# Optimization experiments

Hardware: AMD Instinct MI355X
Metric: run time of the kernel (lower is better)

Reference implementation:

```python
import jax, jax.numpy as jnp
import numpy as np

T_ROIS = 200                       # TRAIN_ROIS_PER_IMAGE
POS_MAX = int(200 * 0.33)          # 66 max positives
R_RATIO = 1.0 / 0.33               # negative:positive ratio constant
MASK_SIZE = 28
BBOX_STD = np.array([0.1, 0.1, 0.2, 0.2], dtype=np.float32)


def _pairwise_iou(b1, b2):
    # b1 [N,4], b2 [G,4] -> [N,G]
    y1 = jnp.maximum(b1[:, None, 0], b2[None, :, 0])
    x1 = jnp.maximum(b1[:, None, 1], b2[None, :, 1])
    y2 = jnp.minimum(b1[:, None, 2], b2[None, :, 2])
    x2 = jnp.minimum(b1[:, None, 3], b2[None, :, 3])
    inter = jnp.maximum(x2 - x1, 0.0) * jnp.maximum(y2 - y1, 0.0)
    a1 = (b1[:, 2] - b1[:, 0]) * (b1[:, 3] - b1[:, 1])
    a2 = (b2[:, 2] - b2[:, 0]) * (b2[:, 3] - b2[:, 1])
    union = a1[:, None] + a2[None, :] - inter
    return jnp.where(union > 0, inter / jnp.where(union > 0, union, 1.0), 0.0)


def _box_refinement(box, gt):
    h = box[:, 2] - box[:, 0]
    w = box[:, 3] - box[:, 1]
    cy = box[:, 0] + 0.5 * h
    cx = box[:, 1] + 0.5 * w
    gh = gt[:, 2] - gt[:, 0]
    gw = gt[:, 3] - gt[:, 1]
    gcy = gt[:, 0] + 0.5 * gh
    gcx = gt[:, 1] + 0.5 * gw
    return jnp.stack([(gcy - cy) / h, (gcx - cx) / w,
                      jnp.log(gh / h), jnp.log(gw / w)], axis=1)


def _crop_and_resize(images, boxes, size):
    # TF tf.image.crop_and_resize (bilinear, extrapolation 0), images [K,H,W], boxes [K,4]
    K, H, W = images.shape
    y1, x1, y2, x2 = boxes[:, 0], boxes[:, 1], boxes[:, 2], boxes[:, 3]
    i = jnp.arange(size, dtype=images.dtype)
    ys = y1[:, None] * (H - 1) + i[None, :] * ((y2 - y1) * (H - 1) / (size - 1))[:, None]  # [K,S]
    xs = x1[:, None] * (W - 1) + i[None, :] * ((x2 - x1) * (W - 1) / (size - 1))[:, None]
    y0 = jnp.floor(ys)
    x0 = jnp.floor(xs)
    wy = (ys - y0)[:, :, None]   # [K,S,1]
    wx = (xs - x0)[:, None, :]   # [K,1,S]
    y0i = jnp.clip(y0, 0, H - 1).astype(jnp.int32)
    y1i = jnp.clip(y0 + 1, 0, H - 1).astype(jnp.int32)
    x0i = jnp.clip(x0, 0, W - 1).astype(jnp.int32)
    x1i = jnp.clip(x0 + 1, 0, W - 1).astype(jnp.int32)
    kk = jnp.arange(K)[:, None, None]
    v00 = images[kk, y0i[:, :, None], x0i[:, None, :]]
    v01 = images[kk, y0i[:, :, None], x1i[:, None, :]]
    v10 = images[kk, y1i[:, :, None], x0i[:, None, :]]
    v11 = images[kk, y1i[:, :, None], x1i[:, None, :]]
    val = (v00 * (1 - wx) + v01 * wx) * (1 - wy) + (v10 * (1 - wx) + v11 * wx) * wy
    ok = ((ys >= 0) & (ys <= H - 1))[:, :, None] & ((xs >= 0) & (xs <= W - 1))[:, None, :]
    return jnp.where(ok, val, 0.0)


def _detection_targets(proposals, gt_class_ids, gt_boxes, gt_masks):
    # proposals [N,4] f32, gt_class_ids [G] int32, gt_boxes [G,4] f32, gt_masks [H,W,G] bool
    valid_prop = jnp.sum(jnp.abs(proposals), axis=1) > 0          # trim_zeros (as mask)
    valid_gt = jnp.sum(jnp.abs(gt_boxes), axis=1) > 0
    is_crowd = valid_gt & (gt_class_ids < 0)
    is_fg = valid_gt & (gt_class_ids > 0)
    iou = _pairwise_iou(proposals, gt_boxes)                       # [N,G]
    iou = jnp.where(valid_prop[:, None], iou, 0.0)
    crowd_max = jnp.max(jnp.where(is_crowd[None, :], iou, 0.0), axis=1)
    no_crowd = crowd_max < 1e-3
    roi_iou_max = jnp.max(jnp.where(is_fg[None, :], iou, 0.0), axis=1)
    pos_bool = (roi_iou_max >= 0.5) & valid_prop
    neg_bool = (roi_iou_max < 0.5) & no_crowd & valid_prop
    num_pos = jnp.minimum(jnp.sum(pos_bool), POS_MAX)
    num_neg_want = jnp.floor(R_RATIO * num_pos.astype(jnp.float32)).astype(jnp.int32) - num_pos
    num_neg = jnp.clip(jnp.minimum(num_neg_want, jnp.sum(neg_bool)), 0, T_ROIS - num_pos)
    # deterministic subsample: lowest-index positives/negatives first (stable argsort)
    pos_order = jnp.argsort(jnp.logical_not(pos_bool))
    neg_order = jnp.argsort(jnp.logical_not(neg_bool))
    j = jnp.arange(T_ROIS)
    is_p = j < num_pos
    is_n = (j >= num_pos) & (j < num_pos + num_neg)
    sel = jnp.where(is_p, pos_order[j], neg_order[jnp.maximum(j - num_pos, 0)])
    keep = (is_p | is_n).astype(proposals.dtype)
    rois = proposals[sel] * keep[:, None]                          # zero-padded tail
    assign = jnp.argmax(jnp.where(is_fg[None, :], iou, -1.0)[sel], axis=1)
    class_ids = jnp.where(is_p, gt_class_ids[assign], 0)
    dummy = jnp.array([0.0, 0.0, 1.0, 1.0], dtype=proposals.dtype)  # safe box for padded rows
    p_roi = jnp.where(is_p[:, None], rois, dummy)
    p_gt = jnp.where(is_p[:, None], gt_boxes[assign], dummy)
    deltas = _box_refinement(p_roi, p_gt) / jnp.asarray(BBOX_STD)
    deltas = deltas * is_p[:, None]
    # mask targets: only first POS_MAX slots can be positive
    masks_t = jnp.transpose(gt_masks.astype(proposals.dtype), (2, 0, 1))   # [G,H,W]
    roi_m = masks_t[assign[:POS_MAX]]                              # [66,H,W]
    m = _crop_and_resize(roi_m, p_roi[:POS_MAX], MASK_SIZE)
    m = jnp.round(m) * is_p[:POS_MAX, None, None]
    masks = jnp.pad(m, ((0, T_ROIS - POS_MAX), (0, 0), (0, 0)))
    return rois, class_ids, deltas, masks


def _rand_boxes(k, shape):
    yx1 = jax.random.uniform(k, shape + (2,)) * 0.7
    hw = jax.random.uniform(jax.random.fold_in(k, 1), shape + (2,)) * 0.28 + 0.02
    return jnp.stack([yx1[..., 0], yx1[..., 1],
                      yx1[..., 0] + hw[..., 0], yx1[..., 1] + hw[..., 1]], axis=-1)


def setup_inputs() -> dict:
    key = jax.random.key(0)
    ks = jax.random.split(key, 6)
    B, N, G, H, W = 2, 2000, 100, 512, 512
    proposals = _rand_boxes(ks[0], (B, N))
    proposals = proposals * (jnp.arange(N) < int(N * 0.9))[None, :, None]  # zero-padded tail
    gt_boxes = _rand_boxes(ks[1], (B, G))
    gt_valid = jnp.arange(G) < 80
    gt_boxes = gt_boxes * gt_valid[None, :, None]
    cls = jax.random.randint(ks[2], (B, G), 1, 81).astype(jnp.int32)
    crowd = jax.random.uniform(ks[3], (B, G)) < 0.05
    cls = jnp.where(crowd, -cls, cls)
    cls = jnp.where(gt_valid[None, :], cls, 0)
    gt_masks = jax.random.randint(ks[4], (B, H, W, G), 0, 2).astype(bool)
    return {"proposals": proposals, "gt_class_ids": cls,
            "gt_boxes": gt_boxes, "gt_masks": gt_masks}


def reference(proposals, gt_class_ids, gt_boxes, gt_masks):
    return jax.vmap(_detection_targets)(proposals, gt_class_ids, gt_boxes, gt_masks)
```

## Files before the change

### kernel.cpp

```cpp
#include <hip/hip_runtime.h>
#include <math.h>

#define NPROP 2000
#define NGT   100
#define HH    512
#define WW    512
#define TR    200
#define PMAX  66
#define MS    28

__global__ __launch_bounds__(512) void k_select(
    const float* __restrict__ props,
    const int*   __restrict__ gcls,
    const float* __restrict__ gbox,
    float* __restrict__ out,
    int* __restrict__ wsi)
{
    const int b = blockIdx.x;
    const int t = threadIdx.x;
    const float* P  = props + (size_t)b * NPROP * 4;
    const float* GB = gbox  + (size_t)b * NGT * 4;
    const int*   GC = gcls  + (size_t)b * NGT;

    __shared__ float s_gb[NGT][4];
    __shared__ int   s_gc[NGT];
    __shared__ unsigned char s_fg[NGT], s_crowd[NGT];
    __shared__ float s_garea[NGT];
    __shared__ unsigned char s_pos[NPROP], s_neg[NPROP];
    __shared__ short s_assign[NPROP];
    __shared__ int s_selp[PMAX], s_seln[TR];
    __shared__ int s_wp[8], s_wn[8];
    __shared__ int s_totp, s_totn, s_np, s_nn;

    if (t < NGT) {
        float g0 = GB[t*4+0], g1 = GB[t*4+1], g2 = GB[t*4+2], g3 = GB[t*4+3];
        s_gb[t][0]=g0; s_gb[t][1]=g1; s_gb[t][2]=g2; s_gb[t][3]=g3;
        bool vg = (fabsf(g0)+fabsf(g1)+fabsf(g2)+fabsf(g3)) > 0.0f;
        int c = GC[t];
        s_gc[t] = c;
        s_fg[t]    = (unsigned char)(vg && (c > 0));
        s_crowd[t] = (unsigned char)(vg && (c < 0));
        s_garea[t] = __fmul_rn(__fsub_rn(g2,g0), __fsub_rn(g3,g1));
    }
    __syncthreads();

    for (int i = t; i < NPROP; i += 512) {
        float p0=P[i*4+0], p1=P[i*4+1], p2=P[i*4+2], p3=P[i*4+3];
        bool vp = (fabsf(p0)+fabsf(p1)+fabsf(p2)+fabsf(p3)) > 0.0f;
        float a1 = __fmul_rn(__fsub_rn(p2,p0), __fsub_rn(p3,p1));
        float crowd_max = 0.0f;
        float fgmax = 0.0f;
        float best = -INFINITY; int arg = 0;
        for (int g = 0; g < NGT; ++g) {
            float y1 = fmaxf(p0, s_gb[g][0]);
            float x1 = fmaxf(p1, s_gb[g][1]);
            float y2 = fminf(p2, s_gb[g][2]);
            float x2 = fminf(p3, s_gb[g][3]);
            float inter = __fmul_rn(fmaxf(__fsub_rn(x2,x1), 0.0f),
                                    fmaxf(__fsub_rn(y2,y1), 0.0f));
            float un = __fsub_rn(__fadd_rn(a1, s_garea[g]), inter);
            float iou = (un > 0.0f) ? __fdiv_rn(inter, un) : 0.0f;
            if (!vp) iou = 0.0f;
            if (s_crowd[g]) crowd_max = fmaxf(crowd_max, iou);
            float v;
            if (s_fg[g]) { fgmax = fmaxf(fgmax, iou); v = iou; }
            else         { v = -1.0f; }
            if (v > best) { best = v; arg = g; }
        }
        s_pos[i]    = (unsigned char)((fgmax >= 0.5f) && vp);
        s_neg[i]    = (unsigned char)((fgmax < 0.5f) && (crowd_max < 0.001f) && vp);
        s_assign[i] = (short)arg;
    }
    __syncthreads();

    int t4 = t * 4;
    int cp = 0, cn = 0;
    unsigned char lp[4], ln[4];
    #pragma unroll
    for (int e = 0; e < 4; ++e) {
        int i = t4 + e;
        unsigned char p = (i < NPROP) ? s_pos[i] : (unsigned char)0;
        unsigned char n = (i < NPROP) ? s_neg[i] : (unsigned char)0;
        lp[e] = p; ln[e] = n; cp += p; cn += n;
    }
    int ip = cp, inn = cn;
    int lane = t & 63;
    #pragma unroll
    for (int d = 1; d < 64; d <<= 1) {
        int vp2 = __shfl_up(ip, d);
        int vn2 = __shfl_up(inn, d);
        if (lane >= d) { ip += vp2; inn += vn2; }
    }
    if (lane == 63) { s_wp[t >> 6] = ip; s_wn[t >> 6] = inn; }
    __syncthreads();
    if (t == 0) {
        int ap = 0, an = 0;
        for (int w = 0; w < 8; ++w) {
            int tp = s_wp[w]; s_wp[w] = ap; ap += tp;
            int tn = s_wn[w]; s_wn[w] = an; an += tn;
        }
        s_totp = ap; s_totn = an;
    }
    __syncthreads();
    int ep = s_wp[t >> 6] + ip - cp;
    int en = s_wn[t >> 6] + inn - cn;
    #pragma unroll
    for (int e = 0; e < 4; ++e) {
        if (lp[e]) { if (ep < PMAX) s_selp[ep] = t4 + e; ep++; }
        if (ln[e]) { if (en < TR)   s_seln[en] = t4 + e; en++; }
    }
    __syncthreads();

    if (t == 0) {
        int np = min(s_totp, PMAX);
        const float R = (float)(1.0 / 0.33);
        int want = (int)floorf(__fmul_rn(R, (float)np)) - np;
        int nn = min(want, s_totn);
        nn = min(nn, TR - np);
        nn = max(nn, 0);
        s_np = np; s_nn = nn;
        wsi[b] = np;
    }
    __syncthreads();

    if (t < TR) {
        const int j = t;
        const int np = s_np, nn = s_nn;
        const bool isp  = j < np;
        const bool kept = j < np + nn;
        float r0=0, r1=0, r2=0, r3=0, cid=0, d0=0, d1=0, d2=0, d3=0;
        if (kept) {
            int sel = isp ? s_selp[j] : s_seln[j - np];
            r0 = P[sel*4+0]; r1 = P[sel*4+1]; r2 = P[sel*4+2]; r3 = P[sel*4+3];
            if (isp) {
                int g = (int)s_assign[sel];
                cid = (float)s_gc[g];
                float h  = __fsub_rn(r2, r0), w = __fsub_rn(r3, r1);
                float cy = __fadd_rn(r0, __fmul_rn(0.5f, h));
                float cx = __fadd_rn(r1, __fmul_rn(0.5f, w));
                float gh  = __fsub_rn(s_gb[g][2], s_gb[g][0]);
                float gw  = __fsub_rn(s_gb[g][3], s_gb[g][1]);
                float gcy = __fadd_rn(s_gb[g][0], __fmul_rn(0.5f, gh));
                float gcx = __fadd_rn(s_gb[g][1], __fmul_rn(0.5f, gw));
                d0 = __fdiv_rn(__fdiv_rn(__fsub_rn(gcy, cy), h), 0.1f);
                d1 = __fdiv_rn(__fdiv_rn(__fsub_rn(gcx, cx), w), 0.1f);
                d2 = __fdiv_rn(logf(__fdiv_rn(gh, h)), 0.2f);
                d3 = __fdiv_rn(logf(__fdiv_rn(gw, w)), 0.2f);
                if (j < PMAX) {
                    wsi[2 + b*PMAX + j] = g;
                    float* wsf = (float*)(wsi + 2 + 2*PMAX);
                    wsf[(b*PMAX + j)*4 + 0] = r0;
                    wsf[(b*PMAX + j)*4 + 1] = r1;
                    wsf[(b*PMAX + j)*4 + 2] = r2;
                    wsf[(b*PMAX + j)*4 + 3] = r3;
                }
            }
        }
        out[(size_t)b*TR*4 + j*4 + 0] = r0;
        out[(size_t)b*TR*4 + j*4 + 1] = r1;
        out[(size_t)b*TR*4 + j*4 + 2] = r2;
        out[(size_t)b*TR*4 + j*4 + 3] = r3;
        out[1600 + (size_t)b*TR + j] = cid;
        out[2000 + (size_t)b*TR*4 + j*4 + 0] = d0;
        out[2000 + (size_t)b*TR*4 + j*4 + 1] = d1;
        out[2000 + (size_t)b*TR*4 + j*4 + 2] = d2;
        out[2000 + (size_t)b*TR*4 + j*4 + 3] = d3;
    }
}

__global__ __launch_bounds__(256) void k_masks(
    const int* __restrict__ gmask,
    const int* __restrict__ wsi,
    float* __restrict__ out)
{
    const int bid = blockIdx.x;
    const int b = bid / TR, j = bid % TR;
    float* mout = out + 3600 + (size_t)b*TR*MS*MS + (size_t)j*MS*MS;
    const int np = wsi[b];
    if (j >= np) {
        for (int p = threadIdx.x; p < MS*MS; p += 256) mout[p] = 0.0f;
        return;
    }
    const int g = wsi[2 + b*PMAX + j];
    const float* wsf = (const float*)(wsi + 2 + 2*PMAX);
    const float y1 = wsf[(b*PMAX + j)*4 + 0];
    const float x1 = wsf[(b*PMAX + j)*4 + 1];
    const float y2 = wsf[(b*PMAX + j)*4 + 2];
    const float x2 = wsf[(b*PMAX + j)*4 + 3];

    const float sy = __fdiv_rn(__fmul_rn(__fsub_rn(y2, y1), 511.0f), 27.0f);
    const float sx = __fdiv_rn(__fmul_rn(__fsub_rn(x2, x1), 511.0f), 27.0f);
    const float by = __fmul_rn(y1, 511.0f);
    const float bx = __fmul_rn(x1, 511.0f);
    const int* GM = gmask + (size_t)b * HH * WW * NGT + g;

    for (int p = threadIdx.x; p < MS*MS; p += 256) {
        int iy = p / MS, ix = p % MS;
        float ys = __fadd_rn(by, __fmul_rn((float)iy, sy));
        float xs = __fadd_rn(bx, __fmul_rn((float)ix, sx));
        float y0f = floorf(ys), x0f = floorf(xs);
        float wy = __fsub_rn(ys, y0f);
        float wx = __fsub_rn(xs, x0f);
        int y0i = (int)fminf(fmaxf(y0f, 0.0f), 511.0f);
        int y1i = (int)fminf(fmaxf(__fadd_rn(y0f, 1.0f), 0.0f), 511.0f);
        int x0i = (int)fminf(fmaxf(x0f, 0.0f), 511.0f);
        int x1i = (int)fminf(fmaxf(__fadd_rn(x0f, 1.0f), 0.0f), 511.0f);
        float v00 = (float)GM[((size_t)y0i * WW + x0i) * NGT];
        float v01 = (float)GM[((size_t)y0i * WW + x1i) * NGT];
        float v10 = (float)GM[((size_t)y1i * WW + x0i) * NGT];
        float v11 = (float)GM[((size_t)y1i * WW + x1i) * NGT];
        float omwx = __fsub_rn(1.0f, wx), omwy = __fsub_rn(1.0f, wy);
        float top = __fadd_rn(__fmul_rn(v00, omwx), __fmul_rn(v01, wx));
        float bot = __fadd_rn(__fmul_rn(v10, omwx), __fmul_rn(v11, wx));
        float val = __fadd_rn(__fmul_rn(top, omwy), __fmul_rn(bot, wy));
        bool ok = (ys >= 0.0f) && (ys <= 511.0f) && (xs >= 0.0f) && (xs <= 511.0f);
        val = ok ? val : 0.0f;
        mout[p] = rintf(val);
    }
}

extern "C" void kernel_launch(void* const* d_in, const int* in_sizes, int n_in,
                              void* d_out, int out_size, void* d_ws, size_t ws_size,
                              hipStream_t stream) {
    const float* props = (const float*)d_in[0];
    const int*   gcls  = (const int*)  d_in[1];
    const float* gbox  = (const float*)d_in[2];
    const int*   gmask = (const int*)  d_in[3];
    float* out = (float*)d_out;
    int* wsi = (int*)d_ws;

    k_select<<<2, 512, 0, stream>>>(props, gcls, gbox, out, wsi);
    k_masks<<<2 * TR, 256, 0, stream>>>(gmask, wsi, out);
}
```

Before: 325.9 us.

## Split IoU flag computation into a separate multi-block kernel before selection

The per-proposal IoU and flag computation moves out of the 2-block select kernel into a new kernel launched on an 8x2 grid of 256-thread blocks. Each proposal's pos/neg flags and assigned GT index are packed into one int in workspace. A smaller pick kernel then reads these flags to run the scan and compaction, and reads GT boxes and classes from global memory. This spreads the 100-GT IoU loop over 16 blocks instead of 2, at the cost of one extra kernel launch and a workspace round-trip.

```diff
diff --git a/kernel.cpp b/kernel.cpp
--- a/kernel.cpp
+++ b/kernel.cpp
@@ -8,8 +8,64 @@
 #define TR    200
 #define PMAX  66
 #define MS    28
-
-__global__ __launch_bounds__(512) void k_select(
+#define FLAGS_OFF 4096
+
+__global__ __launch_bounds__(256) void k_flags(
+    const float* __restrict__ props,
+    const int*   __restrict__ gcls,
+    const float* __restrict__ gbox,
+    int* __restrict__ wsi)
+{
+    const int b = blockIdx.y;
+    const int i = blockIdx.x * 256 + threadIdx.x;
+    const float* P  = props + (size_t)b * NPROP * 4;
+    const float* GB = gbox  + (size_t)b * NGT * 4;
+    const int*   GC = gcls  + (size_t)b * NGT;
+
+    __shared__ float s_gb[NGT][4];
+    __shared__ float s_garea[NGT];
+    __shared__ unsigned char s_fg[NGT], s_crowd[NGT];
+
+    if (threadIdx.x < NGT) {
+        int t = threadIdx.x;
+        float g0 = GB[t*4+0], g1 = GB[t*4+1], g2 = GB[t*4+2], g3 = GB[t*4+3];
+        s_gb[t][0]=g0; s_gb[t][1]=g1; s_gb[t][2]=g2; s_gb[t][3]=g3;
+        bool vg = (fabsf(g0)+fabsf(g1)+fabsf(g2)+fabsf(g3)) > 0.0f;
+        int c = GC[t];
+        s_fg[t]    = (unsigned char)(vg && (c > 0));
+        s_crowd[t] = (unsigned char)(vg && (c < 0));
+        s_garea[t] = __fmul_rn(__fsub_rn(g2,g0), __fsub_rn(g3,g1));
+    }
+    __syncthreads();
+
+    if (i >= NPROP) return;
+    float p0=P[i*4+0], p1=P[i*4+1], p2=P[i*4+2], p3=P[i*4+3];
+    bool vp = (fabsf(p0)+fabsf(p1)+fabsf(p2)+fabsf(p3)) > 0.0f;
+    float a1 = __fmul_rn(__fsub_rn(p2,p0), __fsub_rn(p3,p1));
+    float crowd_max = 0.0f, fgmax = 0.0f;
+    float best = -INFINITY; int arg = 0;
+    for (int g = 0; g < NGT; ++g) {
+        float y1 = fmaxf(p0, s_gb[g][0]);
+        float x1 = fmaxf(p1, s_gb[g][1]);
+        float y2 = fminf(p2, s_gb[g][2]);
+        float x2 = fminf(p3, s_gb[g][3]);
+        float inter = __fmul_rn(fmaxf(__fsub_rn(x2,x1), 0.0f),
+                                fmaxf(__fsub_rn(y2,y1), 0.0f));
+        float un = __fsub_rn(__fadd_rn(a1, s_garea[g]), inter);
+        float iou = (un > 0.0f) ? __fdiv_rn(inter, un) : 0.0f;
+        if (!vp) iou = 0.0f;
+        if (s_crowd[g]) crowd_max = fmaxf(crowd_max, iou);
+        float v;
+        if (s_fg[g]) { fgmax = fmaxf(fgmax, iou); v = iou; }
+        else         { v = -1.0f; }
+        if (v > best) { best = v; arg = g; }
+    }
+    int pos = (int)((fgmax >= 0.5f) && vp);
+    int neg = (int)((fgmax < 0.5f) && (crowd_max < 0.001f) && vp);
+    wsi[FLAGS_OFF + b*NPROP + i] = pos | (neg << 1) | (arg << 2);
+}
+
+__global__ __launch_bounds__(512) void k_pick(
     const float* __restrict__ props,
     const int*   __restrict__ gcls,
     const float* __restrict__ gbox,
@@ -21,67 +77,19 @@
     const float* P  = props + (size_t)b * NPROP * 4;
     const float* GB = gbox  + (size_t)b * NGT * 4;
     const int*   GC = gcls  + (size_t)b * NGT;
-
-    __shared__ float s_gb[NGT][4];
-    __shared__ int   s_gc[NGT];
-    __shared__ unsigned char s_fg[NGT], s_crowd[NGT];
-    __shared__ float s_garea[NGT];
-    __shared__ unsigned char s_pos[NPROP], s_neg[NPROP];
-    __shared__ short s_assign[NPROP];
-    __shared__ int s_selp[PMAX], s_seln[TR];
+    const int*   F  = wsi + FLAGS_OFF + b * NPROP;
+
+    __shared__ int s_selp[PMAX], s_seln[TR], s_selpg[PMAX];
     __shared__ int s_wp[8], s_wn[8];
     __shared__ int s_totp, s_totn, s_np, s_nn;
 
-    if (t < NGT) {
-        float g0 = GB[t*4+0], g1 = GB[t*4+1], g2 = GB[t*4+2], g3 = GB[t*4+3];
-        s_gb[t][0]=g0; s_gb[t][1]=g1; s_gb[t][2]=g2; s_gb[t][3]=g3;
-        bool vg = (fabsf(g0)+fabsf(g1)+fabsf(g2)+fabsf(g3)) > 0.0f;
-        int c = GC[t];
-        s_gc[t] = c;
-        s_fg[t]    = (unsigned char)(vg && (c > 0));
-        s_crowd[t] = (unsigned char)(vg && (c < 0));
-        s_garea[t] = __fmul_rn(__fsub_rn(g2,g0), __fsub_rn(g3,g1));
-    }
-    __syncthreads();
-
-    for (int i = t; i < NPROP; i += 512) {
-        float p0=P[i*4+0], p1=P[i*4+1], p2=P[i*4+2], p3=P[i*4+3];
-        bool vp = (fabsf(p0)+fabsf(p1)+fabsf(p2)+fabsf(p3)) > 0.0f;
-        float a1 = __fmul_rn(__fsub_rn(p2,p0), __fsub_rn(p3,p1));
-        float crowd_max = 0.0f;
-        float fgmax = 0.0f;
-        float best = -INFINITY; int arg = 0;
-        for (int g = 0; g < NGT; ++g) {
-            float y1 = fmaxf(p0, s_gb[g][0]);
-            float x1 = fmaxf(p1, s_gb[g][1]);
-            float y2 = fminf(p2, s_gb[g][2]);
-            float x2 = fminf(p3, s_gb[g][3]);
-            float inter = __fmul_rn(fmaxf(__fsub_rn(x2,x1), 0.0f),
-                                    fmaxf(__fsub_rn(y2,y1), 0.0f));
-            float un = __fsub_rn(__fadd_rn(a1, s_garea[g]), inter);
-            float iou = (un > 0.0f) ? __fdiv_rn(inter, un) : 0.0f;
-            if (!vp) iou = 0.0f;
-            if (s_crowd[g]) crowd_max = fmaxf(crowd_max, iou);
-            float v;
-            if (s_fg[g]) { fgmax = fmaxf(fgmax, iou); v = iou; }
-            else         { v = -1.0f; }
-            if (v > best) { best = v; arg = g; }
-        }
-        s_pos[i]    = (unsigned char)((fgmax >= 0.5f) && vp);
-        s_neg[i]    = (unsigned char)((fgmax < 0.5f) && (crowd_max < 0.001f) && vp);
-        s_assign[i] = (short)arg;
-    }
-    __syncthreads();
-
     int t4 = t * 4;
-    int cp = 0, cn = 0;
-    unsigned char lp[4], ln[4];
+    int fl[4]; int cp = 0, cn = 0;
     #pragma unroll
     for (int e = 0; e < 4; ++e) {
         int i = t4 + e;
-        unsigned char p = (i < NPROP) ? s_pos[i] : (unsigned char)0;
-        unsigned char n = (i < NPROP) ? s_neg[i] : (unsigned char)0;
-        lp[e] = p; ln[e] = n; cp += p; cn += n;
+        fl[e] = (i < NPROP) ? F[i] : 0;
+        cp += (fl[e] & 1); cn += ((fl[e] >> 1) & 1);
     }
     int ip = cp, inn = cn;
     int lane = t & 63;
@@ -106,8 +114,8 @@
     int en = s_wn[t >> 6] + inn - cn;
     #pragma unroll
     for (int e = 0; e < 4; ++e) {
-        if (lp[e]) { if (ep < PMAX) s_selp[ep] = t4 + e; ep++; }
-        if (ln[e]) { if (en < TR)   s_seln[en] = t4 + e; en++; }
+        if (fl[e] & 1) { if (ep < PMAX) { s_selp[ep] = t4 + e; s_selpg[ep] = (fl[e] >> 2) & 127; } ep++; }
+        if ((fl[e] >> 1) & 1) { if (en < TR) s_seln[en] = t4 + e; en++; }
     }
     __syncthreads();
 
@@ -133,15 +141,16 @@
             int sel = isp ? s_selp[j] : s_seln[j - np];
             r0 = P[sel*4+0]; r1 = P[sel*4+1]; r2 = P[sel*4+2]; r3 = P[sel*4+3];
             if (isp) {
-                int g = (int)s_assign[sel];
-                cid = (float)s_gc[g];
+                int g = s_selpg[j];
+                cid = (float)GC[g];
+                float gb0 = GB[g*4+0], gb1 = GB[g*4+1], gb2 = GB[g*4+2], gb3 = GB[g*4+3];
                 float h  = __fsub_rn(r2, r0), w = __fsub_rn(r3, r1);
                 float cy = __fadd_rn(r0, __fmul_rn(0.5f, h));
                 float cx = __fadd_rn(r1, __fmul_rn(0.5f, w));
-                float gh  = __fsub_rn(s_gb[g][2], s_gb[g][0]);
-                float gw  = __fsub_rn(s_gb[g][3], s_gb[g][1]);
-                float gcy = __fadd_rn(s_gb[g][0], __fmul_rn(0.5f, gh));
-                float gcx = __fadd_rn(s_gb[g][1], __fmul_rn(0.5f, gw));
+                float gh  = __fsub_rn(gb2, gb0);
+                float gw  = __fsub_rn(gb3, gb1);
+                float gcy = __fadd_rn(gb0, __fmul_rn(0.5f, gh));
+                float gcx = __fadd_rn(gb1, __fmul_rn(0.5f, gw));
                 d0 = __fdiv_rn(__fdiv_rn(__fsub_rn(gcy, cy), h), 0.1f);
                 d1 = __fdiv_rn(__fdiv_rn(__fsub_rn(gcx, cx), w), 0.1f);
                 d2 = __fdiv_rn(logf(__fdiv_rn(gh, h)), 0.2f);
@@ -229,6 +238,8 @@
     float* out = (float*)d_out;
     int* wsi = (int*)d_ws;
 
-    k_select<<<2, 512, 0, stream>>>(props, gcls, gbox, out, wsi);
+    dim3 gA(8, 2);
+    k_flags<<<gA, 256, 0, stream>>>(props, gcls, gbox, wsi);
+    k_pick<<<2, 512, 0, stream>>>(props, gcls, gbox, out, wsi);
     k_masks<<<2 * TR, 256, 0, stream>>>(gmask, wsi, out);
 }
```

Result: faster. 276.5 us (-15.1%).
